# Performance work log

Hardware: AMD Instinct MI355X
Metric: run time of the kernel (lower is better)

## Reference

```python
import jax, jax.numpy as jnp
import numpy as np
from jax import lax

B, C, H, W = 8, 256, 64, 64
HEADS = 8
STRIDE = 2


def _grouped_conv(x, w, b, stride, groups):
    # x: [B, Cin, H, W]; w: [Cout, Cin/groups, k, k] (OIHW)
    y = lax.conv_general_dilated(x, w, (stride, stride), 'VALID',
                                 dimension_numbers=('NCHW', 'OIHW', 'NCHW'),
                                 feature_group_count=groups)
    return y + b[None, :, None, None]


def _grouped_conv_transpose(x, w, b, stride, groups):
    # Equivalent of torch ConvTranspose2d(kernel=stride, stride=stride, groups=groups)
    # implemented as lhs-dilated conv. w: [Cout, Cin/groups, k, k] (already in conv-equivalent layout).
    k = w.shape[-1]
    pad = k - 1
    y = lax.conv_general_dilated(x, w, (1, 1), [(pad, pad), (pad, pad)],
                                 lhs_dilation=(stride, stride),
                                 dimension_numbers=('NCHW', 'OIHW', 'NCHW'),
                                 feature_group_count=groups)
    return y + b[None, :, None, None]


def setup_inputs() -> dict:
    key = jax.random.key(0)
    ks = jax.random.split(key, 12)
    s = 0.05
    inp = {
        'q': jax.random.normal(ks[0], (B, C, H, W), jnp.float32),
        'k': jax.random.normal(ks[1], (B, C, H, W), jnp.float32),
        'v': jax.random.normal(ks[2], (B, C, H, W), jnp.float32),
        # grouped QKV conv weights: groups=C, out=C*HEADS -> [C*HEADS, 1, s, s]
        'wq': jax.random.normal(ks[3], (C * HEADS, 1, STRIDE, STRIDE), jnp.float32) * s,
        'bq': jax.random.normal(ks[4], (C * HEADS,), jnp.float32) * s,
        'wk': jax.random.normal(ks[5], (C * HEADS, 1, STRIDE, STRIDE), jnp.float32) * s,
        'bk': jax.random.normal(ks[6], (C * HEADS,), jnp.float32) * s,
        'wv': jax.random.normal(ks[7], (C * HEADS, 1, STRIDE, STRIDE), jnp.float32) * s,
        'bv': jax.random.normal(ks[8], (C * HEADS,), jnp.float32) * s,
        # deconv (groups=C, in=C*HEADS, out=C) in conv-equivalent OIHW layout: [C, HEADS, s, s]
        'wo': jax.random.normal(ks[9], (C, HEADS, STRIDE, STRIDE), jnp.float32) * s,
        'bo': jax.random.normal(ks[10], (C,), jnp.float32) * s,
        'gamma': jax.random.normal(ks[11], (1,), jnp.float32),
    }
    return inp


def reference(q, k, v, wq, bq, wk, bk, wv, bv, wo, bo, gamma):
    Bn, Cq, Hq, Wsp = q.shape
    Ckv = k.shape[1]
    # grouped conv projections -> [B, heads, C, L]
    pq = _grouped_conv(q, wq, bq, STRIDE, Cq).reshape(Bn, HEADS, Cq, -1)
    pk = _grouped_conv(k, wk, bk, STRIDE, Ckv).reshape(Bn, HEADS, Ckv, -1)
    pv = _grouped_conv(v, wv, bv, STRIDE, Ckv).reshape(Bn, HEADS, Ckv, -1)
    scale = pq.shape[3] ** (-0.5)
    # channel-wise attention: [B, h, Cq, Ckv]
    attn = jax.nn.softmax(jnp.einsum('bhcl,bhdl->bhcd', pq, pk) * scale, axis=-1)
    out = jnp.einsum('bhcd,bhdl->bhcl', attn, pv)  # [B, h, Cq, L]
    out = out.reshape(Bn, HEADS * Cq, Hq // STRIDE, Wsp // STRIDE)
    out = _grouped_conv_transpose(out, wo, bo, STRIDE, Cq)  # [B, Cq, Hq, Wsp]
    # dropout is identity at inference
    return q + out * gamma
```

## Files before the change

kernel.cpp:

```cpp
#include <hip/hip_runtime.h>
#include <hip/hip_bf16.h>

typedef __bf16 bf16;
typedef __bf16 bf16x4 __attribute__((ext_vector_type(4)));
typedef __bf16 bf16x8 __attribute__((ext_vector_type(8)));
typedef float f32x4 __attribute__((ext_vector_type(4)));
typedef long i64;

__device__ __forceinline__ void gload16(const void* g, void* l) {
  __builtin_amdgcn_global_load_lds(
      (const __attribute__((address_space(1))) unsigned int*)g,
      (__attribute__((address_space(3))) unsigned int*)l, 16, 0, 0);
}


__global__ __launch_bounds__(256) void proj_kqv(
    const float* __restrict__ kin, const float* __restrict__ qin,
    const float* __restrict__ vin,
    const float* __restrict__ wk, const float* __restrict__ bk,
    const float* __restrict__ wq, const float* __restrict__ bq,
    const float* __restrict__ wv, const float* __restrict__ bv,
    char* __restrict__ Pk, char* __restrict__ Pq, char* __restrict__ Vt) {
  int b = blockIdx.y;
  int x = blockIdx.x;
  int t = threadIdx.x;
  int wave = t >> 6, lane = t & 63;
  __shared__ __attribute__((aligned(16))) char smem[32768];
  if (x < 256) {
    bool isq = x >= 128;
    int g0 = (x & 127)*2;
    const float* in   = isq ? qin : kin;
    const float* w    = isq ? wq : wk;
    const float* bias = isq ? bq : bk;
    char* out         = isq ? Pq : Pk;
    int j = (t >> 3) & 7, n = t & 7;
    float4 wv0 = reinterpret_cast<const float4*>(w)[g0*8 + j];
    float  bb0 = bias[g0*8 + j];
    float4 wv1 = reinterpret_cast<const float4*>(w)[g0*8 + 8 + j];
    float  bb1 = bias[g0*8 + 8 + j];
    __builtin_amdgcn_sched_barrier(0);
    const char* s0 = (const char*)(in + ((size_t)b*256 + g0)*4096) + wave*4096 + lane*16;
    char* d0 = smem + wave*4096;
    char* d1 = smem + 16384 + wave*4096;
#pragma unroll
    for (int i = 0; i < 4; i++) gload16(s0 + i*1024, d0 + i*1024);
    __builtin_amdgcn_sched_barrier(0);
#pragma unroll
    for (int i = 0; i < 4; i++) gload16(s0 + 16384 + i*1024, d1 + i*1024);
    __builtin_amdgcn_sched_barrier(0);
    int h = g0 >> 5;
    int bh = b*8 + h;

#define CONVST(bufp, g, wvv, bj) { \
    const float* chf = reinterpret_cast<const float*>(bufp); \
    int c0l = ((g) & 31)*8; \
    _Pragma("unroll") \
    for (int p = 0; p < 4; p++) { \
      int kb = p*4 + wave; \
      int m = kb*2 + (n >> 2); \
      int n0 = (n & 3)*8; \
      float rr0[16], rr1[16]; \
      const float4* R0 = reinterpret_cast<const float4*>(chf + (2*m)*64 + 2*n0); \
      const float4* R1 = reinterpret_cast<const float4*>(chf + (2*m+1)*64 + 2*n0); \
      _Pragma("unroll") \
      for (int u = 0; u < 4; u++) { \
        *reinterpret_cast<float4*>(rr0 + u*4) = R0[u]; \
        *reinterpret_cast<float4*>(rr1 + u*4) = R1[u]; \
      } \
      float ov[8]; \
      _Pragma("unroll") \
      for (int u = 0; u < 8; u++) \
        ov[u] = (bj) + (wvv).x*rr0[2*u] + (wvv).y*rr0[2*u+1] + (wvv).z*rr1[2*u] + (wvv).w*rr1[2*u+1]; \
      int w0 = 0, w1 = 0; \
      w0 = __builtin_amdgcn_cvt_pk_fp8_f32(ov[0], ov[1], w0, false); \
      w0 = __builtin_amdgcn_cvt_pk_fp8_f32(ov[2], ov[3], w0, true); \
      w1 = __builtin_amdgcn_cvt_pk_fp8_f32(ov[4], ov[5], w1, false); \
      w1 = __builtin_amdgcn_cvt_pk_fp8_f32(ov[6], ov[7], w1, true); \
      size_t off = (((size_t)bh*16 + kb)*256 + c0l + j)*64 + (size_t)((n ^ j)*8); \
      int2 st; st.x = w0; st.y = w1; \
      *reinterpret_cast<int2*>(out + off) = st; \
    } }

    asm volatile("s_waitcnt vmcnt(4)" ::: "memory");
    __builtin_amdgcn_s_barrier();
    CONVST(smem, g0, wv0, bb0);
    __builtin_amdgcn_sched_barrier(0);
    asm volatile("s_waitcnt vmcnt(4)" ::: "memory");
    __builtin_amdgcn_s_barrier();
    CONVST(smem + 16384, g0 + 1, wv1, bb1);
#undef CONVST
  } else {
    float* ch = reinterpret_cast<float*>(smem);
    int r = x - 256;
    int m = r & 31, h = r >> 5;
    {
      int seg = t >> 2, part = t & 3;
      int gl = seg >> 1, ky = seg & 1;
      const float* src = vin + (((size_t)b*256 + h*32 + gl)*64 + (2*m + ky))*64;
      float* drow = ch + (gl*2 + ky)*67;
#pragma unroll
      for (int i = 0; i < 4; i++) {
        float4 v = reinterpret_cast<const float4*>(src)[part + i*4];
        int x0 = (part + i*4)*4;
        drow[x0]=v.x; drow[x0+1]=v.y; drow[x0+2]=v.z; drow[x0+3]=v.w;
      }
    }
    int cgrp = t & 31, lgr = t >> 5;
    int c0 = cgrp*8;
    float4 wv8[8]; float bb8[8];
#pragma unroll
    for (int u = 0; u < 8; u++) {
      wv8[u] = reinterpret_cast<const float4*>(wv)[h*256 + c0 + u];
      bb8[u] = bv[h*256 + c0 + u];
    }
    __syncthreads();
    const float* r0 = ch + (cgrp*2 + 0)*67;
    const float* r1 = ch + (cgrp*2 + 1)*67;
    int bh = b*8 + h;
    char* base = Vt + ((size_t)bh*4 + (c0 >> 6))*65536;
    int gsw = ((cgrp & 7) ^ lgr)*8;
#pragma unroll
    for (int p = 0; p < 4; p++) {
      int n = p*8 + lgr;
      int l = m*32 + n;
      float c00 = r0[2*n], c01 = r0[2*n+1], c10 = r1[2*n], c11 = r1[2*n+1];
      float ov[8];
#pragma unroll
      for (int u = 0; u < 8; u++)
        ov[u] = 8.f*(bb8[u] + wv8[u].x*c00 + wv8[u].y*c01 + wv8[u].z*c10 + wv8[u].w*c11);
      int w0 = 0, w1 = 0;
      w0 = __builtin_amdgcn_cvt_pk_fp8_f32(ov[0], ov[1], w0, false);
      w0 = __builtin_amdgcn_cvt_pk_fp8_f32(ov[2], ov[3], w0, true);
      w1 = __builtin_amdgcn_cvt_pk_fp8_f32(ov[4], ov[5], w1, false);
      w1 = __builtin_amdgcn_cvt_pk_fp8_f32(ov[6], ov[7], w1, true);
      int2 st; st.x = w0; st.y = w1;
      *reinterpret_cast<int2*>(base + (size_t)l*64 + gsw) = st;
    }
  }
}

__global__ __launch_bounds__(256, 2) void attn_qk(
    const char* __restrict__ Pq, const char* __restrict__ Pk,
    char* __restrict__ Pattn) {
  int raw = blockIdx.x;
  int idx = raw >> 3;
  int bh = (raw & 7)*8 + (idx >> 2);
  int cs = idx & 3;
  int t = threadIdx.x, wave = t >> 6, lane = t & 63, lg = lane >> 4, lr = lane & 15;
  __shared__ __attribute__((aligned(16))) char smem[40960];
  char* Kb0 = smem;
  char* Kb1 = smem + 16384;
  char* Qb0 = smem + 32768;
  char* Qb1 = smem + 36864;
  float (*red)[64] = reinterpret_cast<float (*)[64]>(smem + 32768);
  char* Pst = smem;
  const char* Kbase = Pk + (size_t)bh*262144 + wave*4096 + lane*16;
  const char* Qbase = Pq + (size_t)bh*262144 + (size_t)cs*4096 + wave*1024 + lane*16;
  char* Kd0 = Kb0 + wave*4096;  char* Kd1 = Kb1 + wave*4096;
  char* Qd0 = Qb0 + wave*1024;  char* Qd1 = Qb1 + wave*1024;

#define STAGE(kb, K_, Q_) { \
    const char* kc = Kbase + (size_t)(kb)*16384; \
    _Pragma("unroll") \
    for (int i_ = 0; i_ < 4; i_++) gload16(kc + i_*1024, (K_) + i_*1024); \
    gload16(Qbase + (size_t)(kb)*16384, (Q_)); }

  f32x4 acc[4][4];
#pragma unroll
  for (int i = 0; i < 4; i++)
#pragma unroll
    for (int j = 0; j < 4; j++) { f32x4 z = {0.f,0.f,0.f,0.f}; acc[i][j] = z; }

  STAGE(0, Kd0, Qd0);
#pragma unroll
  for (int kb = 0; kb < 16; kb++) {
    if (kb < 15) {
      if (kb & 1) { STAGE(kb+1, Kd0, Qd0); } else { STAGE(kb+1, Kd1, Qd1); }
      asm volatile("s_waitcnt vmcnt(5)" ::: "memory");
    } else {
      asm volatile("s_waitcnt vmcnt(0)" ::: "memory");
    }
    __builtin_amdgcn_s_barrier();
    __builtin_amdgcn_sched_barrier(0);
    const char* Kc = (kb & 1) ? Kb1 : Kb0;
    const char* Qc = (kb & 1) ? Qb1 : Qb0;
#pragma unroll
    for (int ks = 0; ks < 2; ks++) {
      int colx = (ks*32 + lg*8) ^ ((lr & 7) << 3);
      i64 a[4];
#pragma unroll
      for (int mi = 0; mi < 4; mi++)
        a[mi] = *reinterpret_cast<const i64*>(Qc + (mi*16 + lr)*64 + colx);
#pragma unroll
      for (int ni = 0; ni < 4; ni++) {
        i64 bfr = *reinterpret_cast<const i64*>(Kc + (wave*64 + ni*16 + lr)*64 + colx);
#pragma unroll
        for (int mi = 0; mi < 4; mi++)
          acc[mi][ni] = __builtin_amdgcn_mfma_f32_16x16x32_fp8_fp8(a[mi], bfr, acc[mi][ni], 0, 0, 0);
      }
    }
    __builtin_amdgcn_s_barrier();
    __builtin_amdgcn_sched_barrier(0);
  }
#undef STAGE
  const float scale = 0.03125f;
  float sums[4][4];
#pragma unroll
  for (int mi = 0; mi < 4; mi++)
#pragma unroll
    for (int r = 0; r < 4; r++) {
      float mx = fmaxf(fmaxf(acc[mi][0][r], acc[mi][1][r]), fmaxf(acc[mi][2][r], acc[mi][3][r]));
#pragma unroll
      for (int off = 1; off < 16; off <<= 1) mx = fmaxf(mx, __shfl_xor(mx, off, 64));
      red[wave][mi*16 + lg*4 + r] = mx;
    }
  __syncthreads();
#pragma unroll
  for (int mi = 0; mi < 4; mi++)
#pragma unroll
    for (int r = 0; r < 4; r++) {
      int clr = mi*16 + lg*4 + r;
      float mx = fmaxf(fmaxf(red[0][clr], red[1][clr]), fmaxf(red[2][clr], red[3][clr]));
      float s = 0.f;
#pragma unroll
      for (int ni = 0; ni < 4; ni++) {
        float p = __expf(scale*(acc[mi][ni][r] - mx));
        acc[mi][ni][r] = p; s += p;
      }
#pragma unroll
      for (int off = 1; off < 16; off <<= 1) s += __shfl_xor(s, off, 64);
      sums[mi][r] = s;
    }
  __syncthreads();
#pragma unroll
  for (int mi = 0; mi < 4; mi++)
#pragma unroll
    for (int r = 0; r < 4; r++) red[wave][mi*16 + lg*4 + r] = sums[mi][r];
  __syncthreads();
#pragma unroll
  for (int mi = 0; mi < 4; mi++)
#pragma unroll
    for (int r = 0; r < 4; r++) {
      int clr = mi*16 + lg*4 + r;
      float iv = 32.f/(red[0][clr] + red[1][clr] + red[2][clr] + red[3][clr]);
      char* prow = Pst + wave*4096 + clr*64;
      int xr = (clr & 7) << 3;
#pragma unroll
      for (int ni = 0; ni < 4; ni += 2) {
        int pk2 = __builtin_amdgcn_cvt_pk_fp8_f32(acc[mi][ni][r]*iv, acc[mi][ni+1][r]*iv, 0, false);
        prow[(ni*16 + lr) ^ xr]     = (char)(pk2 & 0xff);
        prow[((ni+1)*16 + lr) ^ xr] = (char)((pk2 >> 8) & 0xff);
      }
    }
  __syncthreads();
  const uint4* ls = reinterpret_cast<const uint4*>(Pst);
#pragma unroll
  for (int i = 0; i < 4; i++) {
    int f = i*256 + t;
    int kb = f >> 8, rem = f & 255;
    char* dst = Pattn + ((size_t)(bh*4 + kb)*256 + cs*64)*64 + (size_t)rem*16;
    *reinterpret_cast<uint4*>(dst) = ls[f];
  }
}

__global__ __launch_bounds__(256, 4) void pv_deconv(const char* __restrict__ Pattn,
    const char* __restrict__ Vt, const float* __restrict__ qin,
    const float* __restrict__ wo, const float* __restrict__ bo,
    const float* __restrict__ gamma, float* __restrict__ outp) {
  int raw = blockIdx.x;
  int idx = raw >> 3;
  int pair = (raw & 7)*32 + (idx >> 2);
  int tb = idx & 3;
  int mb = pair & 3, bh = pair >> 2;
  int h = bh & 7, b = bh >> 3;
  int t = threadIdx.x, wave = t >> 6, lane = t & 63, lg = lane >> 4, lr = lane & 15;
  __shared__ __attribute__((aligned(16))) char smem[40960];
  char* Pl   = smem;
  char* Vl   = smem + 4096;
  bf16* OlT  = reinterpret_cast<bf16*>(smem);
  float* wo_s = reinterpret_cast<float*>(smem + 36864);
  float* bo_s = reinterpret_cast<float*>(smem + 37888);
  const char* Pbase = Pattn + (size_t)bh*65536 + tb*4096;
  const char* Vbase = Vt + (size_t)bh*262144 + mb*16384;
  f32x4 acc[4][4];
#pragma unroll
  for (int i = 0; i < 4; i++)
#pragma unroll
    for (int j = 0; j < 4; j++) { f32x4 z = {0.f,0.f,0.f,0.f}; acc[i][j] = z; }
  for (int kb = 0; kb < 4; kb++) {
    __syncthreads();
    {
      const char* pc = Pbase + (size_t)kb*16384 + wave*1024 + lane*16;
      gload16(pc, Pl + wave*1024);
      const char* vc = Vbase + (size_t)kb*65536 + wave*4096 + lane*16;
      char* vl = Vl + wave*4096;
#pragma unroll
      for (int i = 0; i < 4; i++) gload16(vc + i*1024, vl + i*1024);
    }
    __syncthreads();
#pragma unroll
    for (int ks = 0; ks < 2; ks++) {
      int colx = (ks*32 + lg*8) ^ ((lr & 7) << 3);
      i64 a[4];
#pragma unroll
      for (int mi = 0; mi < 4; mi++)
        a[mi] = *reinterpret_cast<const i64*>(Pl + (mi*16 + lr)*64 + colx);
#pragma unroll
      for (int ni = 0; ni < 4; ni++) {
        i64 bfr = *reinterpret_cast<const i64*>(Vl + (wave*64 + ni*16 + lr)*64 + colx);
#pragma unroll
        for (int mi = 0; mi < 4; mi++)
          acc[mi][ni] = __builtin_amdgcn_mfma_f32_16x16x32_fp8_fp8(a[mi], bfr, acc[mi][ni], 0, 0, 0);
      }
    }
  }
  __syncthreads();
  const float rescale = 1.f/256.f;
#pragma unroll
  for (int mi = 0; mi < 4; mi++)
#pragma unroll
    for (int ni = 0; ni < 4; ni++) {
      int l = wave*64 + ni*16 + lr;
      int cb = mi*16 + lg*4;
      bf16x4 p;
      p[0] = (bf16)(acc[mi][ni][0]*rescale); p[1] = (bf16)(acc[mi][ni][1]*rescale);
      p[2] = (bf16)(acc[mi][ni][2]*rescale); p[3] = (bf16)(acc[mi][ni][3]*rescale);
      *reinterpret_cast<bf16x4*>(OlT + l*66 + cb) = p;
    }
  wo_s[t] = wo[((size_t)(h*32 + tb*8 + (t>>5)))*32 + (t & 31)];
  if (t < 8) bo_s[t] = bo[h*32 + tb*8 + t];
  __syncthreads();
  int xq = t & 15, b5 = (t >> 4) & 1, ct = t >> 5;
  float2 wp[8];
#pragma unroll
  for (int j = 0; j < 8; j++)
    wp[j] = *reinterpret_cast<const float2*>(wo_s + ct*32 + j*4 + (1 - b5)*2);
  float bias = bo_s[ct];
  float gm = gamma[0];
  int co = h*32 + tb*8 + ct;
#pragma unroll
  for (int it = 0; it < 8; it++) {
    int y = it*2 + b5;
    int ll0 = it*32 + xq*2;
    bf16x4 o00 = *reinterpret_cast<const bf16x4*>(OlT + ll0*66 + ct*8);
    bf16x4 o01 = *reinterpret_cast<const bf16x4*>(OlT + ll0*66 + ct*8 + 4);
    bf16x4 o10 = *reinterpret_cast<const bf16x4*>(OlT + (ll0+1)*66 + ct*8);
    bf16x4 o11 = *reinterpret_cast<const bf16x4*>(OlT + (ll0+1)*66 + ct*8 + 4);
    float v0 = bias, v1 = bias, v2 = bias, v3 = bias;
#pragma unroll
    for (int j = 0; j < 4; j++) {
      float f0 = (float)o00[j], f1 = (float)o01[j];
      v0 += f0*wp[j].y;   v1 += f0*wp[j].x;
      v0 += f1*wp[4+j].y; v1 += f1*wp[4+j].x;
      float g0 = (float)o10[j], g1 = (float)o11[j];
      v2 += g0*wp[j].y;   v3 += g0*wp[j].x;
      v2 += g1*wp[4+j].y; v3 += g1*wp[4+j].x;
    }
    size_t oi = (((size_t)b*256 + co)*64 + (mb*16 + y))*64 + xq*4;
    float4 qv = *reinterpret_cast<const float4*>(qin + oi);
    float4 ov;
    ov.x = qv.x + gm*v0; ov.y = qv.y + gm*v1;
    ov.z = qv.z + gm*v2; ov.w = qv.w + gm*v3;
    *reinterpret_cast<float4*>(outp + oi) = ov;
  }
}

extern "C" void kernel_launch(void* const* d_in, const int* in_sizes, int n_in,
                              void* d_out, int out_size, void* d_ws, size_t ws_size,
                              hipStream_t stream) {
  const float* q  = (const float*)d_in[0];
  const float* k  = (const float*)d_in[1];
  const float* v  = (const float*)d_in[2];
  const float* wq = (const float*)d_in[3];
  const float* bq = (const float*)d_in[4];
  const float* wk = (const float*)d_in[5];
  const float* bk = (const float*)d_in[6];
  const float* wv = (const float*)d_in[7];
  const float* bv = (const float*)d_in[8];
  const float* wo = (const float*)d_in[9];
  const float* bo = (const float*)d_in[10];
  const float* gamma = (const float*)d_in[11];
  float* out = (float*)d_out;

  char* ws = (char*)d_ws;
  char* Pk    = ws;
  char* Pq    = ws + 16777216;
  char* Vt    = ws + 33554432;
  char* Pattn = ws + 50331648;

  proj_kqv<<<dim3(512, 8), 256, 0, stream>>>(k, q, v, wk, bk, wq, bq, wv, bv, Pk, Pq, Vt);
  attn_qk <<<dim3(256), 256, 0, stream>>>(Pq, Pk, Pattn);
  pv_deconv<<<dim3(1024), 256, 0, stream>>>(Pattn, Vt, q, wo, bo, gamma, out);
}
```

Baseline: 69.51 us.

## Double-buffer half-channel staging in QK projection to cut LDS and overlap loads

Splits each channel's staging into half-channel chunks held in two 8KB LDS buffers. Loads for later halves are issued while earlier halves are being convolved, and each wave reads only the rows it loaded itself, so the block barriers are removed. This shrinks shared memory per block (helping occupancy) and overlaps global loads with compute. The cost is finer-grained waitcnt management that must stay correct for LDS reuse. The else branch also uses smem and needs to fit in the smaller buffer.

```diff
diff --git a/kernel.cpp b/kernel.cpp
--- a/kernel.cpp
+++ b/kernel.cpp
@@ -25,7 +25,7 @@
   int x = blockIdx.x;
   int t = threadIdx.x;
   int wave = t >> 6, lane = t & 63;
-  __shared__ __attribute__((aligned(16))) char smem[32768];
+  __shared__ __attribute__((aligned(16))) char smem[17152];
   if (x < 256) {
     bool isq = x >= 128;
     int g0 = (x & 127)*2;
@@ -39,33 +39,30 @@
     float4 wv1 = reinterpret_cast<const float4*>(w)[g0*8 + 8 + j];
     float  bb1 = bias[g0*8 + 8 + j];
     __builtin_amdgcn_sched_barrier(0);
-    const char* s0 = (const char*)(in + ((size_t)b*256 + g0)*4096) + wave*4096 + lane*16;
-    char* d0 = smem + wave*4096;
-    char* d1 = smem + 16384 + wave*4096;
-#pragma unroll
-    for (int i = 0; i < 4; i++) gload16(s0 + i*1024, d0 + i*1024);
-    __builtin_amdgcn_sched_barrier(0);
-#pragma unroll
-    for (int i = 0; i < 4; i++) gload16(s0 + 16384 + i*1024, d1 + i*1024);
+    const char* src = (const char*)(in + ((size_t)b*256 + g0)*4096) + wave*2048 + lane*16;
+    char* bw0 = smem + wave*2048;
+    char* bw1 = smem + 8192 + wave*2048;
+#define STAGEH(i, dst) { const char* s_ = src + ((i)>>1)*16384 + ((i)&1)*8192; \
+    gload16(s_, dst); gload16(s_ + 1024, (dst) + 1024); }
+    STAGEH(0, bw0);
+    STAGEH(1, bw1);
     __builtin_amdgcn_sched_barrier(0);
     int h = g0 >> 5;
     int bh = b*8 + h;
-
-#define CONVST(bufp, g, wvv, bj) { \
-    const float* chf = reinterpret_cast<const float*>(bufp); \
-    int c0l = ((g) & 31)*8; \
+    int colb = (n & 3)*64;
+    int rsel = 2*(n >> 2);
+
+#define CONVH(i, bufwp, wvv, bj) { \
+    int c0l = ((g0 + ((i)>>1)) & 31)*8; \
     _Pragma("unroll") \
-    for (int p = 0; p < 4; p++) { \
-      int kb = p*4 + wave; \
-      int m = kb*2 + (n >> 2); \
-      int n0 = (n & 3)*8; \
+    for (int pp = 0; pp < 2; pp++) { \
+      int kb = ((i)&1)*8 + wave*2 + pp; \
+      const char* R0p = (bufwp) + (pp*4 + rsel)*256 + colb; \
       float rr0[16], rr1[16]; \
-      const float4* R0 = reinterpret_cast<const float4*>(chf + (2*m)*64 + 2*n0); \
-      const float4* R1 = reinterpret_cast<const float4*>(chf + (2*m+1)*64 + 2*n0); \
       _Pragma("unroll") \
       for (int u = 0; u < 4; u++) { \
-        *reinterpret_cast<float4*>(rr0 + u*4) = R0[u]; \
-        *reinterpret_cast<float4*>(rr1 + u*4) = R1[u]; \
+        *reinterpret_cast<float4*>(rr0 + u*4) = *reinterpret_cast<const float4*>(R0p + u*16); \
+        *reinterpret_cast<float4*>(rr1 + u*4) = *reinterpret_cast<const float4*>(R0p + 256 + u*16); \
       } \
       float ov[8]; \
       _Pragma("unroll") \
@@ -81,14 +78,24 @@
       *reinterpret_cast<int2*>(out + off) = st; \
     } }
 
+    asm volatile("s_waitcnt vmcnt(2)" ::: "memory");
+    CONVH(0, bw0, wv0, bb0);
+    asm volatile("s_waitcnt lgkmcnt(0)" ::: "memory");
+    __builtin_amdgcn_sched_barrier(0);
+    STAGEH(2, bw0);
+    __builtin_amdgcn_sched_barrier(0);
     asm volatile("s_waitcnt vmcnt(4)" ::: "memory");
-    __builtin_amdgcn_s_barrier();
-    CONVST(smem, g0, wv0, bb0);
+    CONVH(1, bw1, wv0, bb0);
+    asm volatile("s_waitcnt lgkmcnt(0)" ::: "memory");
+    __builtin_amdgcn_sched_barrier(0);
+    STAGEH(3, bw1);
     __builtin_amdgcn_sched_barrier(0);
     asm volatile("s_waitcnt vmcnt(4)" ::: "memory");
-    __builtin_amdgcn_s_barrier();
-    CONVST(smem + 16384, g0 + 1, wv1, bb1);
-#undef CONVST
+    CONVH(2, bw0, wv1, bb1);
+    asm volatile("s_waitcnt vmcnt(2)" ::: "memory");
+    CONVH(3, bw1, wv1, bb1);
+#undef CONVH
+#undef STAGEH
   } else {
     float* ch = reinterpret_cast<float*>(smem);
     int r = x - 256;
```

Result: no change. 69.34 us (-0.2%).

## Load Q/K projection inputs directly to registers, dropping LDS staging

Applied to the files above, without the earlier changes.

The K/Q projection branch no longer stages two input channels through LDS with async global-to-LDS loads and barriers. Each thread now reads its 2x32-float input patch straight from global memory into registers and computes all 8 head outputs from that patch, reusing the loaded data across heads. This removes LDS traffic and barriers and shrinks the shared-memory allocation, which can raise occupancy. In exchange, the Q/K branch issues more global reads per thread and uses more registers, and it loses the explicit load/compute overlap.

```diff
diff --git a/kernel.cpp b/kernel.cpp
--- a/kernel.cpp
+++ b/kernel.cpp
@@ -24,8 +24,7 @@
   int b = blockIdx.y;
   int x = blockIdx.x;
   int t = threadIdx.x;
-  int wave = t >> 6, lane = t & 63;
-  __shared__ __attribute__((aligned(16))) char smem[32768];
+  __shared__ __attribute__((aligned(16))) char smem[17152];
   if (x < 256) {
     bool isq = x >= 128;
     int g0 = (x & 127)*2;
@@ -33,62 +32,42 @@
     const float* w    = isq ? wq : wk;
     const float* bias = isq ? bq : bk;
     char* out         = isq ? Pq : Pk;
-    int j = (t >> 3) & 7, n = t & 7;
-    float4 wv0 = reinterpret_cast<const float4*>(w)[g0*8 + j];
-    float  bb0 = bias[g0*8 + j];
-    float4 wv1 = reinterpret_cast<const float4*>(w)[g0*8 + 8 + j];
-    float  bb1 = bias[g0*8 + 8 + j];
-    __builtin_amdgcn_sched_barrier(0);
-    const char* s0 = (const char*)(in + ((size_t)b*256 + g0)*4096) + wave*4096 + lane*16;
-    char* d0 = smem + wave*4096;
-    char* d1 = smem + 16384 + wave*4096;
-#pragma unroll
-    for (int i = 0; i < 4; i++) gload16(s0 + i*1024, d0 + i*1024);
-    __builtin_amdgcn_sched_barrier(0);
-#pragma unroll
-    for (int i = 0; i < 4; i++) gload16(s0 + 16384 + i*1024, d1 + i*1024);
-    __builtin_amdgcn_sched_barrier(0);
-    int h = g0 >> 5;
-    int bh = b*8 + h;
-
-#define CONVST(bufp, g, wvv, bj) { \
-    const float* chf = reinterpret_cast<const float*>(bufp); \
-    int c0l = ((g) & 31)*8; \
-    _Pragma("unroll") \
-    for (int p = 0; p < 4; p++) { \
-      int kb = p*4 + wave; \
-      int m = kb*2 + (n >> 2); \
-      int n0 = (n & 3)*8; \
-      float rr0[16], rr1[16]; \
-      const float4* R0 = reinterpret_cast<const float4*>(chf + (2*m)*64 + 2*n0); \
-      const float4* R1 = reinterpret_cast<const float4*>(chf + (2*m+1)*64 + 2*n0); \
-      _Pragma("unroll") \
-      for (int u = 0; u < 4; u++) { \
-        *reinterpret_cast<float4*>(rr0 + u*4) = R0[u]; \
-        *reinterpret_cast<float4*>(rr1 + u*4) = R1[u]; \
-      } \
-      float ov[8]; \
-      _Pragma("unroll") \
-      for (int u = 0; u < 8; u++) \
-        ov[u] = (bj) + (wvv).x*rr0[2*u] + (wvv).y*rr0[2*u+1] + (wvv).z*rr1[2*u] + (wvv).w*rr1[2*u+1]; \
-      int w0 = 0, w1 = 0; \
-      w0 = __builtin_amdgcn_cvt_pk_fp8_f32(ov[0], ov[1], w0, false); \
-      w0 = __builtin_amdgcn_cvt_pk_fp8_f32(ov[2], ov[3], w0, true); \
-      w1 = __builtin_amdgcn_cvt_pk_fp8_f32(ov[4], ov[5], w1, false); \
-      w1 = __builtin_amdgcn_cvt_pk_fp8_f32(ov[6], ov[7], w1, true); \
-      size_t off = (((size_t)bh*16 + kb)*256 + c0l + j)*64 + (size_t)((n ^ j)*8); \
-      int2 st; st.x = w0; st.y = w1; \
-      *reinterpret_cast<int2*>(out + off) = st; \
-    } }
-
-    asm volatile("s_waitcnt vmcnt(4)" ::: "memory");
-    __builtin_amdgcn_s_barrier();
-    CONVST(smem, g0, wv0, bb0);
-    __builtin_amdgcn_sched_barrier(0);
-    asm volatile("s_waitcnt vmcnt(4)" ::: "memory");
-    __builtin_amdgcn_s_barrier();
-    CONVST(smem + 16384, g0 + 1, wv1, bb1);
-#undef CONVST
+    int ch = t >> 7, kb = (t >> 3) & 15, gcol = t & 7;
+    int g = g0 + ch;
+    float4 wj[8]; float bj[8];
+#pragma unroll
+    for (int j = 0; j < 8; j++) {
+      wj[j] = reinterpret_cast<const float4*>(w)[g*8 + j];
+      bj[j] = bias[g*8 + j];
+    }
+    const char* chg = (const char*)(in + ((size_t)b*256 + g)*4096);
+    int m = kb*2 + (gcol >> 2);
+    int cb = (gcol & 3)*64;
+    const float4* R0 = reinterpret_cast<const float4*>(chg + (2*m)*256 + cb);
+    const float4* R1 = reinterpret_cast<const float4*>(chg + (2*m+1)*256 + cb);
+    float f0[16], f1[16];
+#pragma unroll
+    for (int u = 0; u < 4; u++) {
+      *reinterpret_cast<float4*>(f0 + u*4) = R0[u];
+      *reinterpret_cast<float4*>(f1 + u*4) = R1[u];
+    }
+    int bh = b*8 + (g >> 5);
+    int c0l = (g & 31)*8;
+    char* rowbase = out + (((size_t)bh*16 + kb)*256 + c0l)*64;
+#pragma unroll
+    for (int j = 0; j < 8; j++) {
+      float ov[8];
+#pragma unroll
+      for (int u = 0; u < 8; u++)
+        ov[u] = bj[j] + wj[j].x*f0[2*u] + wj[j].y*f0[2*u+1] + wj[j].z*f1[2*u] + wj[j].w*f1[2*u+1];
+      int w0 = 0, w1 = 0;
+      w0 = __builtin_amdgcn_cvt_pk_fp8_f32(ov[0], ov[1], w0, false);
+      w0 = __builtin_amdgcn_cvt_pk_fp8_f32(ov[2], ov[3], w0, true);
+      w1 = __builtin_amdgcn_cvt_pk_fp8_f32(ov[4], ov[5], w1, false);
+      w1 = __builtin_amdgcn_cvt_pk_fp8_f32(ov[6], ov[7], w1, true);
+      int2 st; st.x = w0; st.y = w1;
+      *reinterpret_cast<int2*>(rowbase + j*64 + ((gcol ^ j)*8)) = st;
+    }
   } else {
     float* ch = reinterpret_cast<float*>(smem);
     int r = x - 256;
```

Result: no change. 69.70 us (+0.3%).
